# Kernel optimization log

Measured on AMD Instinct MI355X. Metric: run time of the kernel, lower is better.

The kernel has to match this reference:

```python
import jax, jax.numpy as jnp
import numpy as np

E = 128   # embedding_dim
H = 8     # num_attention_heads
D = 16    # head_size = E // H


def setup_inputs() -> dict:
    key = jax.random.key(0)
    ks = jax.random.split(key, 7)
    B, N = 2, 512
    x = jax.random.normal(ks[0], (B, N, E), jnp.float32)
    e = jax.random.uniform(ks[1], (B, N, N), jnp.float32)  # dense pairwise edge weights
    s_qkv = 1.0 / np.sqrt(D)
    w_qkv = jax.random.uniform(ks[2], (3 * H * D, E), jnp.float32, -s_qkv, s_qkv)
    w_ekv = jax.random.normal(ks[3], (2 * H * D, 1), jnp.float32) * 1.0
    b_ekv = jax.random.normal(ks[4], (2 * H * D,), jnp.float32) * 0.01
    s_prj = 1.0 / np.sqrt(E)
    w_prj = jax.random.uniform(ks[5], (E, H * D), jnp.float32, -s_prj, s_prj)
    b_prj = jnp.zeros((E,), jnp.float32)
    return {"x": x, "e": e, "w_qkv": w_qkv, "w_ekv": w_ekv,
            "b_ekv": b_ekv, "w_prj": w_prj, "b_prj": b_prj}


def reference(x, e, w_qkv, w_ekv, b_ekv, w_prj, b_prj):
    B, N, _ = x.shape
    # qkv projection: [B,N,3*H*D] split per einops '(S H D)'
    qkv = (x @ w_qkv.T).reshape(B, N, 3, H, D)
    q = jnp.transpose(qkv[:, :, 0], (0, 2, 1, 3))  # [B,H,N,D]
    k = jnp.transpose(qkv[:, :, 1], (0, 2, 1, 3))  # [B,H,N,D]
    v = jnp.transpose(qkv[:, :, 2], (0, 2, 1, 3))  # [B,H,N,D]
    # edge-conditioned K/V biases: Linear(1 -> 2HD) + LeakyReLU(0.01)
    ekv = jax.nn.leaky_relu(e[..., None] * w_ekv[:, 0] + b_ekv)  # [B,N,M,2HD]
    ekv = ekv.reshape(B, N, N, 2, H, D)
    ekm = jnp.transpose(ekv[..., 0, :, :], (0, 3, 1, 2, 4))  # [B,H,N,M,D]
    evm = jnp.transpose(ekv[..., 1, :, :], (0, 3, 1, 2, 4))  # [B,H,N,M,D]
    # dots[b,h,n,m] = q[b,h,n] . (k[b,h,n] + ekm[b,h,n,m])
    # NOTE: original uses the key of the *query* node n (broadcast over m).
    dots = jnp.sum(q * k, axis=-1)[..., None] \
        + jnp.einsum('bhnd,bhnmd->bhnm', q, ekm)
    attn = jax.nn.softmax(dots / np.sqrt(D), axis=-1)  # [B,H,N,M]
    # hat[b,h,n] = sum_m attn * (v[b,h,n] + evm[b,h,n,m])
    hat = v * jnp.sum(attn, axis=-1)[..., None] \
        + jnp.einsum('bhnm,bhnmd->bhnd', attn, evm)  # [B,H,N,D]
    out = jnp.transpose(hat, (0, 2, 1, 3)).reshape(B, N, H * D) @ w_prj.T + b_prj
    return out
```

## Files before the change

### kernel.cpp

```cpp
#include <hip/hip_runtime.h>
#include <math.h>

#define BATCH 2
#define NSEQ  512
#define EDIM  128
#define HNUM  8
#define DDIM  16
#define MROWS (BATCH*NSEQ)

__global__ __launch_bounds__(256)
void qv_gemm(const float* __restrict__ x, const float* __restrict__ w,
             float* __restrict__ qv) {
    __shared__ float4 As[32 * 32];
    __shared__ float4 Bs[64 * 32];

    const int tid  = threadIdx.x;
    const int row0 = blockIdx.y * 32;
    const int bx   = blockIdx.x;
    const int wr0  = (bx >> 1) * 256 + (bx & 1) * 64;
    const int cc0  = (bx >> 1) * 128 + (bx & 1) * 64;

    #pragma unroll
    for (int it = 0; it < 4; ++it) {
        int idx = tid + it * 256;
        int r = idx >> 5, k4 = idx & 31;
        As[r * 32 + (k4 ^ ((r >> 2) & 7))] =
            ((const float4*)(x + (size_t)(row0 + r) * 128))[k4];
    }
    #pragma unroll
    for (int it = 0; it < 8; ++it) {
        int idx = tid + it * 256;
        int r = idx >> 5, k4 = idx & 31;
        Bs[r * 32 + (k4 ^ ((r >> 2) & 7))] =
            ((const float4*)(w + (size_t)(wr0 + r) * 128))[k4];
    }
    __syncthreads();

    const int ty  = tid >> 4;
    const int tx  = tid & 15;
    const int ra  = ty * 2;
    const int swa = (ra >> 2) & 7;
    const int rb  = tx * 4;
    const int swb = tx & 7;

    float acc[2][4] = {};
    #pragma unroll
    for (int k4 = 0; k4 < 32; ++k4) {
        float4 a0 = As[ ra      * 32 + (k4 ^ swa)];
        float4 a1 = As[(ra + 1) * 32 + (k4 ^ swa)];
        float4 bv4[4];
        #pragma unroll
        for (int j = 0; j < 4; ++j)
            bv4[j] = Bs[(rb + j) * 32 + (k4 ^ swb)];
        #pragma unroll
        for (int j = 0; j < 4; ++j) {
            acc[0][j] = fmaf(a0.x, bv4[j].x, acc[0][j]);
            acc[0][j] = fmaf(a0.y, bv4[j].y, acc[0][j]);
            acc[0][j] = fmaf(a0.z, bv4[j].z, acc[0][j]);
            acc[0][j] = fmaf(a0.w, bv4[j].w, acc[0][j]);
            acc[1][j] = fmaf(a1.x, bv4[j].x, acc[1][j]);
            acc[1][j] = fmaf(a1.y, bv4[j].y, acc[1][j]);
            acc[1][j] = fmaf(a1.z, bv4[j].z, acc[1][j]);
            acc[1][j] = fmaf(a1.w, bv4[j].w, acc[1][j]);
        }
    }

    #pragma unroll
    for (int i = 0; i < 2; ++i) {
        float* crow = qv + (size_t)(row0 + ra + i) * 256 + cc0 + rb;
        *(float4*)crow = make_float4(acc[i][0], acc[i][1], acc[i][2], acc[i][3]);
    }
}

__global__ __launch_bounds__(1024)
void attn_proj(const float* __restrict__ qv,   const float* __restrict__ e,
               const float* __restrict__ wekv, const float* __restrict__ bekv,
               const float* __restrict__ wprj, const float* __restrict__ bprj,
               float* __restrict__ out) {
    __shared__ float hat_s[2][EDIM];
    __shared__ float red[16][DDIM][65];

    const int tid  = threadIdx.x;
    const int lane = tid & 63;
    const int wv   = tid >> 6;
    const int h    = __builtin_amdgcn_readfirstlane(wv & 7);
    const int r    = __builtin_amdgcn_readfirstlane(wv >> 3);
    const int bn   = blockIdx.x * 2 + r;

    const float* erow = e + (size_t)bn * NSEQ;
    float4 e0 = ((const float4*)erow)[lane];
    float4 e1 = ((const float4*)erow)[lane + 64];
    float evs[8] = {e0.x, e0.y, e0.z, e0.w, e1.x, e1.y, e1.z, e1.w};

    const float* qrow = qv + (size_t)bn * 256 + h * DDIM;
    const float* vrow = qrow + 128;

    const float SC = 0.25f * 1.44269504088896340736f;

    float wk[DDIM], bk[DDIM], cd[DDIM], wvv[DDIM], bv[DDIM];
    float qwk = 0.f;
    #pragma unroll
    for (int d = 0; d < DDIM; ++d) {
        float q = qrow[d];
        wk[d]  = wekv[h * DDIM + d];
        bk[d]  = bekv[h * DDIM + d];
        wvv[d] = wekv[EDIM + h * DDIM + d];
        bv[d]  = bekv[EDIM + h * DDIM + d];
        qwk    = fmaf(q, wk[d], qwk);
        cd[d]  = 0.495f * SC * q;
    }
    const float Alin = SC * 0.505f * qwk;

    float racc[DDIM];
    #pragma unroll
    for (int d = 0; d < DDIM; ++d) racc[d] = 0.f;
    float sp = 0.f, spe = 0.f;
    #pragma unroll
    for (int c = 0; c < 8; ++c) {
        float s = evs[c];
        float dot = s * Alin;
        #pragma unroll
        for (int d = 0; d < DDIM; ++d) {
            float t = fmaf(s, wk[d], bk[d]);
            dot = fmaf(cd[d], fabsf(t), dot);
        }
        float p = __builtin_amdgcn_exp2f(dot);
        sp  += p;
        spe  = fmaf(p, s, spe);
        #pragma unroll
        for (int d = 0; d < DDIM; ++d) {
            float t = fmaf(s, wvv[d], bv[d]);
            racc[d] = fmaf(p, fabsf(t), racc[d]);
        }
    }

    const int oc  = tid >> 3;
    const int seg = tid & 7;
    const float4* wp = (const float4*)(wprj + (size_t)oc * EDIM + seg * 16);
    float4 w4[4];
    #pragma unroll
    for (int j = 0; j < 4; ++j) w4[j] = wp[j];

    #pragma unroll
    for (int off = 1; off < 64; off <<= 1) {
        sp  += __shfl_xor(sp,  off, 64);
        spe += __shfl_xor(spe, off, 64);
    }

    #pragma unroll
    for (int d = 0; d < DDIM; ++d)
        red[wv][d][lane] = racc[d];
    const int rc = lane & 15, rg = lane >> 4;
    float part = 0.f;
    #pragma unroll
    for (int j = 0; j < 16; ++j)
        part += red[wv][rc][rg * 16 + j];
    part += __shfl_xor(part, 16, 64);
    part += __shfl_xor(part, 32, 64);

    if (lane < DDIM) {
        float wvs = wekv[EDIM + h * DDIM + lane];
        float bvs = bekv[EDIM + h * DDIM + lane];
        float acc = 0.495f * part + 0.505f * fmaf(wvs, spe, bvs * sp);
        hat_s[r][h * DDIM + lane] = vrow[lane] + acc / sp;
    }
    __syncthreads();

    const float4* h0 = (const float4*)(&hat_s[0][seg * 16]);
    const float4* h1 = (const float4*)(&hat_s[1][seg * 16]);
    float s0 = 0.f, s1 = 0.f;
    #pragma unroll
    for (int j = 0; j < 4; ++j) {
        float4 a = w4[j], p0 = h0[j], p1 = h1[j];
        s0 = fmaf(a.x, p0.x, s0); s0 = fmaf(a.y, p0.y, s0);
        s0 = fmaf(a.z, p0.z, s0); s0 = fmaf(a.w, p0.w, s0);
        s1 = fmaf(a.x, p1.x, s1); s1 = fmaf(a.y, p1.y, s1);
        s1 = fmaf(a.z, p1.z, s1); s1 = fmaf(a.w, p1.w, s1);
    }
    #pragma unroll
    for (int off = 1; off < 8; off <<= 1) {
        s0 += __shfl_xor(s0, off, 64);
        s1 += __shfl_xor(s1, off, 64);
    }
    if (seg < 2) {
        float v = (seg ? s1 : s0) + bprj[oc];
        out[(size_t)(blockIdx.x * 2 + seg) * EDIM + oc] = v;
    }
}

extern "C" void kernel_launch(void* const* d_in, const int* in_sizes, int n_in,
                              void* d_out, int out_size, void* d_ws, size_t ws_size,
                              hipStream_t stream) {
    const float* x     = (const float*)d_in[0];
    const float* e     = (const float*)d_in[1];
    const float* w_qkv = (const float*)d_in[2];
    const float* w_ekv = (const float*)d_in[3];
    const float* b_ekv = (const float*)d_in[4];
    const float* w_prj = (const float*)d_in[5];
    const float* b_prj = (const float*)d_in[6];
    float* out = (float*)d_out;

    float* qv = (float*)d_ws;

    qv_gemm<<<dim3(4, MROWS / 32), 256, 0, stream>>>(x, w_qkv, qv);

    attn_proj<<<MROWS / 2, 1024, 0, stream>>>(qv, e, w_ekv, b_ekv,
                                              w_prj, b_prj, out);
}
```

Measured before the change: 84.99 us.

## Fuse QV projection GEMM into attention kernel, four rows per block

Removes the separate qv_gemm launch and computes the q and v projections inside the attention kernel. Each block loads four x rows into shared memory and reduces against rows of w_qkv held in registers, then runs the edge-attention and output projection for two row pairs in a loop. Edge rows are prefetched before the projection to overlap their loads. This trades a kernel launch and the workspace round trip for redundant reading of w_qkv by every block (256 blocks each reading 256x128 weights) and a longer serial body per block.

```diff
diff --git a/kernel.cpp b/kernel.cpp
--- a/kernel.cpp
+++ b/kernel.cpp
@@ -8,76 +8,14 @@
 #define DDIM  16
 #define MROWS (BATCH*NSEQ)
 
-__global__ __launch_bounds__(256)
-void qv_gemm(const float* __restrict__ x, const float* __restrict__ w,
-             float* __restrict__ qv) {
-    __shared__ float4 As[32 * 32];
-    __shared__ float4 Bs[64 * 32];
-
-    const int tid  = threadIdx.x;
-    const int row0 = blockIdx.y * 32;
-    const int bx   = blockIdx.x;
-    const int wr0  = (bx >> 1) * 256 + (bx & 1) * 64;
-    const int cc0  = (bx >> 1) * 128 + (bx & 1) * 64;
-
-    #pragma unroll
-    for (int it = 0; it < 4; ++it) {
-        int idx = tid + it * 256;
-        int r = idx >> 5, k4 = idx & 31;
-        As[r * 32 + (k4 ^ ((r >> 2) & 7))] =
-            ((const float4*)(x + (size_t)(row0 + r) * 128))[k4];
-    }
-    #pragma unroll
-    for (int it = 0; it < 8; ++it) {
-        int idx = tid + it * 256;
-        int r = idx >> 5, k4 = idx & 31;
-        Bs[r * 32 + (k4 ^ ((r >> 2) & 7))] =
-            ((const float4*)(w + (size_t)(wr0 + r) * 128))[k4];
-    }
-    __syncthreads();
-
-    const int ty  = tid >> 4;
-    const int tx  = tid & 15;
-    const int ra  = ty * 2;
-    const int swa = (ra >> 2) & 7;
-    const int rb  = tx * 4;
-    const int swb = tx & 7;
-
-    float acc[2][4] = {};
-    #pragma unroll
-    for (int k4 = 0; k4 < 32; ++k4) {
-        float4 a0 = As[ ra      * 32 + (k4 ^ swa)];
-        float4 a1 = As[(ra + 1) * 32 + (k4 ^ swa)];
-        float4 bv4[4];
-        #pragma unroll
-        for (int j = 0; j < 4; ++j)
-            bv4[j] = Bs[(rb + j) * 32 + (k4 ^ swb)];
-        #pragma unroll
-        for (int j = 0; j < 4; ++j) {
-            acc[0][j] = fmaf(a0.x, bv4[j].x, acc[0][j]);
-            acc[0][j] = fmaf(a0.y, bv4[j].y, acc[0][j]);
-            acc[0][j] = fmaf(a0.z, bv4[j].z, acc[0][j]);
-            acc[0][j] = fmaf(a0.w, bv4[j].w, acc[0][j]);
-            acc[1][j] = fmaf(a1.x, bv4[j].x, acc[1][j]);
-            acc[1][j] = fmaf(a1.y, bv4[j].y, acc[1][j]);
-            acc[1][j] = fmaf(a1.z, bv4[j].z, acc[1][j]);
-            acc[1][j] = fmaf(a1.w, bv4[j].w, acc[1][j]);
-        }
-    }
-
-    #pragma unroll
-    for (int i = 0; i < 2; ++i) {
-        float* crow = qv + (size_t)(row0 + ra + i) * 256 + cc0 + rb;
-        *(float4*)crow = make_float4(acc[i][0], acc[i][1], acc[i][2], acc[i][3]);
-    }
-}
-
 __global__ __launch_bounds__(1024)
-void attn_proj(const float* __restrict__ qv,   const float* __restrict__ e,
-               const float* __restrict__ wekv, const float* __restrict__ bekv,
-               const float* __restrict__ wprj, const float* __restrict__ bprj,
-               float* __restrict__ out) {
-    __shared__ float hat_s[2][EDIM];
+void attn_all(const float* __restrict__ x,    const float* __restrict__ e,
+              const float* __restrict__ wqkv, const float* __restrict__ wekv,
+              const float* __restrict__ bekv, const float* __restrict__ wprj,
+              const float* __restrict__ bprj, float* __restrict__ out) {
+    __shared__ float xs[4][EDIM];
+    __shared__ float qvs[4][256];
+    __shared__ float hat_s[2][2][EDIM];
     __shared__ float red[16][DDIM][65];
 
     const int tid  = threadIdx.x;
@@ -85,106 +23,148 @@
     const int wv   = tid >> 6;
     const int h    = __builtin_amdgcn_readfirstlane(wv & 7);
     const int r    = __builtin_amdgcn_readfirstlane(wv >> 3);
-    const int bn   = blockIdx.x * 2 + r;
+    const int bn0  = blockIdx.x * 4;
 
-    const float* erow = e + (size_t)bn * NSEQ;
-    float4 e0 = ((const float4*)erow)[lane];
-    float4 e1 = ((const float4*)erow)[lane + 64];
-    float evs[8] = {e0.x, e0.y, e0.z, e0.w, e1.x, e1.y, e1.z, e1.w};
+    const float* er0 = e + (size_t)(bn0 + r)     * NSEQ;
+    const float* er1 = e + (size_t)(bn0 + 2 + r) * NSEQ;
+    float4 epre[2][2];
+    epre[0][0] = ((const float4*)er0)[lane];
+    epre[0][1] = ((const float4*)er0)[lane + 64];
+    epre[1][0] = ((const float4*)er1)[lane];
+    epre[1][1] = ((const float4*)er1)[lane + 64];
 
-    const float* qrow = qv + (size_t)bn * 256 + h * DDIM;
-    const float* vrow = qrow + 128;
+    if (tid < 128) {
+        int rr = tid >> 5, c4 = tid & 31;
+        ((float4*)xs[rr])[c4] = ((const float4*)(x + (size_t)(bn0 + rr) * EDIM))[c4];
+    }
+    __syncthreads();
+
+    {
+        const int oc   = tid >> 2;
+        const int seg  = tid & 3;
+        const int wrow = (oc < 128) ? oc : oc + 128;
+        const float4* wp = (const float4*)(wqkv + (size_t)wrow * EDIM + seg * 32);
+        float4 wreg[8];
+        #pragma unroll
+        for (int j = 0; j < 8; ++j) wreg[j] = wp[j];
+        #pragma unroll
+        for (int rr = 0; rr < 4; ++rr) {
+            const float4* xp = (const float4*)(xs[rr] + seg * 32);
+            float s = 0.f;
+            #pragma unroll
+            for (int j = 0; j < 8; ++j) {
+                float4 w4 = wreg[j], x4 = xp[j];
+                s = fmaf(w4.x, x4.x, s); s = fmaf(w4.y, x4.y, s);
+                s = fmaf(w4.z, x4.z, s); s = fmaf(w4.w, x4.w, s);
+            }
+            s += __shfl_xor(s, 1, 64);
+            s += __shfl_xor(s, 2, 64);
+            if (seg == 0) qvs[rr][oc] = s;
+        }
+    }
+
+    const int oc8  = tid >> 3;
+    const int seg8 = tid & 7;
+    const float4* wpp = (const float4*)(wprj + (size_t)oc8 * EDIM + seg8 * 16);
+    float4 w4[4];
+    #pragma unroll
+    for (int j = 0; j < 4; ++j) w4[j] = wpp[j];
+
+    __syncthreads();
 
     const float SC = 0.25f * 1.44269504088896340736f;
 
-    float wk[DDIM], bk[DDIM], cd[DDIM], wvv[DDIM], bv[DDIM];
-    float qwk = 0.f;
     #pragma unroll
-    for (int d = 0; d < DDIM; ++d) {
-        float q = qrow[d];
-        wk[d]  = wekv[h * DDIM + d];
-        bk[d]  = bekv[h * DDIM + d];
-        wvv[d] = wekv[EDIM + h * DDIM + d];
-        bv[d]  = bekv[EDIM + h * DDIM + d];
-        qwk    = fmaf(q, wk[d], qwk);
-        cd[d]  = 0.495f * SC * q;
-    }
-    const float Alin = SC * 0.505f * qwk;
+    for (int t = 0; t < 2; ++t) {
+        const int row = t * 2 + r;
+        float evs[8] = {epre[t][0].x, epre[t][0].y, epre[t][0].z, epre[t][0].w,
+                        epre[t][1].x, epre[t][1].y, epre[t][1].z, epre[t][1].w};
 
-    float racc[DDIM];
-    #pragma unroll
-    for (int d = 0; d < DDIM; ++d) racc[d] = 0.f;
-    float sp = 0.f, spe = 0.f;
-    #pragma unroll
-    for (int c = 0; c < 8; ++c) {
-        float s = evs[c];
-        float dot = s * Alin;
+        const float* qrow = qvs[row] + h * DDIM;
+        const float* vrow = qvs[row] + 128 + h * DDIM;
+
+        float wk[DDIM], bk[DDIM], cd[DDIM], wvv[DDIM], bv[DDIM];
+        float qwk = 0.f;
         #pragma unroll
         for (int d = 0; d < DDIM; ++d) {
-            float t = fmaf(s, wk[d], bk[d]);
-            dot = fmaf(cd[d], fabsf(t), dot);
+            float q = qrow[d];
+            wk[d]  = wekv[h * DDIM + d];
+            bk[d]  = bekv[h * DDIM + d];
+            wvv[d] = wekv[EDIM + h * DDIM + d];
+            bv[d]  = bekv[EDIM + h * DDIM + d];
+            qwk    = fmaf(q, wk[d], qwk);
+            cd[d]  = 0.495f * SC * q;
         }
-        float p = __builtin_amdgcn_exp2f(dot);
-        sp  += p;
-        spe  = fmaf(p, s, spe);
+        const float Alin = SC * 0.505f * qwk;
+
+        float racc[DDIM];
         #pragma unroll
-        for (int d = 0; d < DDIM; ++d) {
-            float t = fmaf(s, wvv[d], bv[d]);
-            racc[d] = fmaf(p, fabsf(t), racc[d]);
+        for (int d = 0; d < DDIM; ++d) racc[d] = 0.f;
+        float sp = 0.f, spe = 0.f;
+        #pragma unroll
+        for (int c = 0; c < 8; ++c) {
+            float s = evs[c];
+            float dot = s * Alin;
+            #pragma unroll
+            for (int d = 0; d < DDIM; ++d) {
+                float tt = fmaf(s, wk[d], bk[d]);
+                dot = fmaf(cd[d], fabsf(tt), dot);
+            }
+            float p = __builtin_amdgcn_exp2f(dot);
+            sp  += p;
+            spe  = fmaf(p, s, spe);
+            #pragma unroll
+            for (int d = 0; d < DDIM; ++d) {
+                float tt = fmaf(s, wvv[d], bv[d]);
+                racc[d] = fmaf(p, fabsf(tt), racc[d]);
+            }
         }
-    }
 
-    const int oc  = tid >> 3;
-    const int seg = tid & 7;
-    const float4* wp = (const float4*)(wprj + (size_t)oc * EDIM + seg * 16);
-    float4 w4[4];
-    #pragma unroll
-    for (int j = 0; j < 4; ++j) w4[j] = wp[j];
+        #pragma unroll
+        for (int off = 1; off < 64; off <<= 1) {
+            sp  += __shfl_xor(sp,  off, 64);
+            spe += __shfl_xor(spe, off, 64);
+        }
 
-    #pragma unroll
-    for (int off = 1; off < 64; off <<= 1) {
-        sp  += __shfl_xor(sp,  off, 64);
-        spe += __shfl_xor(spe, off, 64);
-    }
+        #pragma unroll
+        for (int d = 0; d < DDIM; ++d)
+            red[wv][d][lane] = racc[d];
+        const int rc = lane & 15, rg = lane >> 4;
+        float part = 0.f;
+        #pragma unroll
+        for (int j = 0; j < 16; ++j)
+            part += red[wv][rc][rg * 16 + j];
+        part += __shfl_xor(part, 16, 64);
+        part += __shfl_xor(part, 32, 64);
 
-    #pragma unroll
-    for (int d = 0; d < DDIM; ++d)
-        red[wv][d][lane] = racc[d];
-    const int rc = lane & 15, rg = lane >> 4;
-    float part = 0.f;
-    #pragma unroll
-    for (int j = 0; j < 16; ++j)
-        part += red[wv][rc][rg * 16 + j];
-    part += __shfl_xor(part, 16, 64);
-    part += __shfl_xor(part, 32, 64);
+        if (lane < DDIM) {
+            float wvs = wekv[EDIM + h * DDIM + lane];
+            float bvs = bekv[EDIM + h * DDIM + lane];
+            float acc = 0.495f * part + 0.505f * fmaf(wvs, spe, bvs * sp);
+            hat_s[t][r][h * DDIM + lane] = vrow[lane] + acc / sp;
+        }
+        __syncthreads();
 
-    if (lane < DDIM) {
-        float wvs = wekv[EDIM + h * DDIM + lane];
-        float bvs = bekv[EDIM + h * DDIM + lane];
-        float acc = 0.495f * part + 0.505f * fmaf(wvs, spe, bvs * sp);
-        hat_s[r][h * DDIM + lane] = vrow[lane] + acc / sp;
-    }
-    __syncthreads();
-
-    const float4* h0 = (const float4*)(&hat_s[0][seg * 16]);
-    const float4* h1 = (const float4*)(&hat_s[1][seg * 16]);
-    float s0 = 0.f, s1 = 0.f;
-    #pragma unroll
-    for (int j = 0; j < 4; ++j) {
-        float4 a = w4[j], p0 = h0[j], p1 = h1[j];
-        s0 = fmaf(a.x, p0.x, s0); s0 = fmaf(a.y, p0.y, s0);
-        s0 = fmaf(a.z, p0.z, s0); s0 = fmaf(a.w, p0.w, s0);
-        s1 = fmaf(a.x, p1.x, s1); s1 = fmaf(a.y, p1.y, s1);
-        s1 = fmaf(a.z, p1.z, s1); s1 = fmaf(a.w, p1.w, s1);
-    }
-    #pragma unroll
-    for (int off = 1; off < 8; off <<= 1) {
-        s0 += __shfl_xor(s0, off, 64);
-        s1 += __shfl_xor(s1, off, 64);
-    }
-    if (seg < 2) {
-        float v = (seg ? s1 : s0) + bprj[oc];
-        out[(size_t)(blockIdx.x * 2 + seg) * EDIM + oc] = v;
+        const float4* h0 = (const float4*)(&hat_s[t][0][seg8 * 16]);
+        const float4* h1 = (const float4*)(&hat_s[t][1][seg8 * 16]);
+        float s0 = 0.f, s1 = 0.f;
+        #pragma unroll
+        for (int j = 0; j < 4; ++j) {
+            float4 a = w4[j], p0 = h0[j], p1 = h1[j];
+            s0 = fmaf(a.x, p0.x, s0); s0 = fmaf(a.y, p0.y, s0);
+            s0 = fmaf(a.z, p0.z, s0); s0 = fmaf(a.w, p0.w, s0);
+            s1 = fmaf(a.x, p1.x, s1); s1 = fmaf(a.y, p1.y, s1);
+            s1 = fmaf(a.z, p1.z, s1); s1 = fmaf(a.w, p1.w, s1);
+        }
+        #pragma unroll
+        for (int off = 1; off < 8; off <<= 1) {
+            s0 += __shfl_xor(s0, off, 64);
+            s1 += __shfl_xor(s1, off, 64);
+        }
+        if (seg8 < 2) {
+            float v = (seg8 ? s1 : s0) + bprj[oc8];
+            out[(size_t)(bn0 + t * 2 + seg8) * EDIM + oc8] = v;
+        }
     }
 }
 
@@ -200,10 +180,6 @@
     const float* b_prj = (const float*)d_in[6];
     float* out = (float*)d_out;
 
-    float* qv = (float*)d_ws;
-
-    qv_gemm<<<dim3(4, MROWS / 32), 256, 0, stream>>>(x, w_qkv, qv);
-
-    attn_proj<<<MROWS / 2, 1024, 0, stream>>>(qv, e, w_ekv, b_ekv,
-                                              w_prj, b_prj, out);
+    attn_all<<<MROWS / 4, 1024, 0, stream>>>(x, e, w_qkv, w_ekv, b_ekv,
+                                             w_prj, b_prj, out);
 }
```

New measurement: 78.97 us. 7.1% less time.
